# Optimization experiments

Measured on AMD Instinct MI355X. Metric: run time of the kernel, lower is better.

Reference implementation:

```python
import jax, jax.numpy as jnp
import numpy as np
import math

B, S, HID, H = 1, 2048, 1024, 16
D = HID // H  # head_dim = 64


def setup_inputs() -> dict:
    key = jax.random.key(0)
    ks = jax.random.split(key, 12)
    s = 0.02
    x = jax.random.normal(ks[0], (B, S, HID), jnp.float32)
    Wq = jax.random.normal(ks[1], (HID, HID), jnp.float32) * s
    bq = jnp.zeros((HID,), jnp.float32)
    Wk = jax.random.normal(ks[2], (HID, HID), jnp.float32) * s
    bk = jnp.zeros((HID,), jnp.float32)
    Wv = jax.random.normal(ks[3], (HID, HID), jnp.float32) * s
    bv = jnp.zeros((HID,), jnp.float32)
    Wo = jax.random.normal(ks[4], (HID, HID), jnp.float32) * s
    bo = jnp.zeros((HID,), jnp.float32)
    # nn.Parameter(torch.ones(3,3)) at init; small noise so the bias is non-degenerate
    cmw = jnp.ones((3, 3), jnp.float32) + 0.1 * jax.random.normal(ks[5], (3, 3), jnp.float32)
    # full causal [B,S,S] mask so the mask.shape[1]==seq_len branch is taken
    mask = jnp.tril(jnp.ones((B, S, S), jnp.int32))
    modality_info = jax.random.randint(ks[6], (B, S), 0, 3, dtype=jnp.int64)
    return dict(x=x, Wq=Wq, bq=bq, Wk=Wk, bk=bk, Wv=Wv, bv=bv, Wo=Wo, bo=bo,
                cmw=cmw, mask=mask, modality_info=modality_info)


def reference(x, Wq, bq, Wk, bk, Wv, bv, Wo, bo, cmw, mask, modality_info):
    b, s, _ = x.shape
    # QKV projections (torch Linear: y = x @ W.T + b), split into heads [B,H,S,D]
    q = (x @ Wq.T + bq).reshape(b, s, H, D).transpose(0, 2, 1, 3)
    k = (x @ Wk.T + bk).reshape(b, s, H, D).transpose(0, 2, 1, 3)
    v = (x @ Wv.T + bv).reshape(b, s, H, D).transpose(0, 2, 1, 3)
    scores = jnp.einsum('bhqd,bhkd->bhqk', q, k) / math.sqrt(D)  # [B,H,S,S]
    # cross-modal bias: gather from 3x3 table via pairwise modality indices -> [B,S,S]
    bias = cmw[modality_info[:, :, None], modality_info[:, None, :]]
    scores = scores + bias[:, None, :, :]  # equals original broadcast when B==1
    scores = jnp.where(mask[:, None, :, :] == 0, -1e9, scores)
    attn = jax.nn.softmax(scores, axis=-1)  # dropout is identity in eval
    ctx = jnp.einsum('bhqk,bhkd->bhqd', attn, v)          # [B,H,S,D]
    ctx = ctx.transpose(0, 2, 1, 3).reshape(b, s, HID)    # [B,S,HID]
    return ctx @ Wo.T + bo
```

## Files before the change

kernel.cpp:

```cpp
#include <hip/hip_runtime.h>
#include <hip/hip_bf16.h>
#include <math.h>

#define S_LEN 2048
#define HID   1024
#define NHEAD 16

using bf16x8 = __attribute__((ext_vector_type(8))) short;
using bf16x4 = __attribute__((ext_vector_type(4))) short;
using f32x4  = __attribute__((ext_vector_type(4))) float;

__device__ __forceinline__ float bf2f(short s) {
  union { unsigned u; float f; } c;
  c.u = ((unsigned)(unsigned short)s) << 16;
  return c.f;
}
__device__ __forceinline__ short f2bf(float f) {
  union { float f; unsigned u; } c; c.f = f;
  unsigned u = c.u;
  unsigned r = (u + 0x7fffu + ((u >> 16) & 1u)) >> 16;
  return (short)r;
}
__device__ __forceinline__ float loadf(const void* base, long idx, int is_bf) {
  return is_bf ? bf2f(((const short*)base)[idx]) : ((const float*)base)[idx];
}
__device__ __forceinline__ void gl_lds16(const void* g, void* l) {
  __builtin_amdgcn_global_load_lds(
      (const __attribute__((address_space(1))) void*)g,
      (__attribute__((address_space(3))) void*)l, 16, 0, 0);
}

__global__ __launch_bounds__(256) void convert5(
    const void* __restrict__ s0, const void* __restrict__ s1, const void* __restrict__ s2,
    const void* __restrict__ s3, const void* __restrict__ s4,
    short* __restrict__ d0, short* __restrict__ d1, short* __restrict__ d2,
    short* __restrict__ d3, short* __restrict__ d4,
    const int* __restrict__ modw, int* __restrict__ flags) {
  __shared__ int sh_isbf;
  const int t = threadIdx.x;

  if (t < 64) {
    const unsigned* xw = (const unsigned*)s0;
    int cnt = 0;
    for (int i = t; i < 1024; i += 64) {
      const unsigned fld = (xw[i] >> 7) & 0xFFu;
      cnt += (fld >= 100u && fld <= 135u) ? 1 : 0;
    }
    for (int m = 1; m < 64; m <<= 1) cnt += __shfl_xor(cnt, m);
    if (t == 0) sh_isbf = (cnt >= 512) ? 1 : 0;
  }
  __syncthreads();
  const int is_bf = sh_isbf;

  if (blockIdx.x == 0 && blockIdx.y == 0 && t < 64) {
    int odd = 0;
    for (int i = 0; i < 4; ++i) {
      const int wv = modw[2 * (t + 64 * i) + 1];
      odd += (wv != 0) ? 1 : 0;
    }
    for (int m = 1; m < 64; m <<= 1) odd += __shfl_xor(odd, m);
    if (t == 0) {
      flags[0] = is_bf;
      flags[1] = (odd == 0) ? 1 : 0;
    }
  }

  const int a = blockIdx.y;
  const void* src = (a == 0) ? s0 : (a == 1) ? s1 : (a == 2) ? s2 : (a == 3) ? s3 : s4;
  short* dst = (a == 0) ? d0 : (a == 1) ? d1 : (a == 2) ? d2 : (a == 3) ? d3 : d4;
  const long n = (a == 0) ? (2L << 20) : (1L << 20);
  long i = (long)(blockIdx.x * 256 + t) * 8;
  const long stride = (long)gridDim.x * 256 * 8;
  if (is_bf) {
    for (; i < n; i += stride)
      *(bf16x8*)(dst + i) = *(const bf16x8*)((const short*)src + i);
  } else {
    for (; i < n; i += stride) {
      const float* p = (const float*)src + i;
      bf16x8 r;
#pragma unroll
      for (int j = 0; j < 8; ++j) r[j] = f2bf(p[j]);
      *(bf16x8*)(dst + i) = r;
    }
  }
}

template <int BM, int BN>
__global__ __launch_bounds__(256) void gemm_bt3(
    const short* __restrict__ A,
    const short* __restrict__ W0, const short* __restrict__ W1, const short* __restrict__ W2,
    const void* __restrict__ b0, const void* __restrict__ b1, const void* __restrict__ b2,
    void* __restrict__ C0, void* __restrict__ C1, void* __restrict__ C2,
    const int* __restrict__ flags, int nbn, int store_f32)
{
  constexpr int K = 1024;
  constexpr int N = 1024;
  constexpr int NKT = K / 64;
  constexpr int WM = (BM == 128) ? 2 : 1;
  constexpr int WN = 4 / WM;
  constexpr int MI = (BM / 16) / WM;
  constexpr int NI = (BN / 16) / WN;
  constexpr int RPA = BM / 16;
  constexpr int RPB = BN / 16;
  __shared__ short As[2][2][BM * 32];
  __shared__ short Bs[2][2][BN * 32];

  const int t = threadIdx.x;
  const int w = t >> 6, lane = t & 63;
  const int l15 = lane & 15, quad = lane >> 4;
  const int wm = w / WN, wn = w % WN;
  const int is_bf = flags[0];

  const int mat = blockIdx.x / nbn;
  const int n0 = (blockIdx.x % nbn) * BN;
  const int m0 = blockIdx.y * BM;

  const short* W  = (mat == 0) ? W0 : (mat == 1 ? W1 : W2);
  const void* bia = (mat == 0) ? b0 : (mat == 1 ? b1 : b2);
  void*       C   = (mat == 0) ? C0 : (mat == 1 ? C1 : C2);

  f32x4 acc[MI][NI];
  for (int mi = 0; mi < MI; ++mi)
    for (int ni = 0; ni < NI; ++ni)
      for (int r = 0; r < 4; ++r) acc[mi][ni][r] = 0.f;

  const int srow = lane >> 2;
  const int sch  = (lane & 3) * 8;

  auto stage = [&](int kt, int buf) {
    for (int g = w; g < 2 * RPA; g += 4) {
      const int p = g / RPA, r0 = (g % RPA) * 16;
      gl_lds16(A + (long)(m0 + r0 + srow) * K + kt * 64 + p * 32 + sch,
               &As[buf][p][r0 * 32]);
    }
    for (int g = w; g < 2 * RPB; g += 4) {
      const int p = g / RPB, r0 = (g % RPB) * 16;
      gl_lds16(W + (long)(n0 + r0 + srow) * K + kt * 64 + p * 32 + sch,
               &Bs[buf][p][r0 * 32]);
    }
  };

  stage(0, 0);
  int cur = 0;
  for (int kt = 0; kt < NKT; ++kt) {
    __syncthreads();
    if (kt + 1 < NKT) stage(kt + 1, cur ^ 1);

    bf16x8 af[MI][2], bfr[NI][2];
    for (int p = 0; p < 2; ++p) {
      for (int mi = 0; mi < MI; ++mi)
        af[mi][p] = *(const bf16x8*)&As[cur][p][(wm * (MI * 16) + mi * 16 + l15) * 32 + quad * 8];
      for (int ni = 0; ni < NI; ++ni)
        bfr[ni][p] = *(const bf16x8*)&Bs[cur][p][(wn * (NI * 16) + ni * 16 + l15) * 32 + quad * 8];
    }
    for (int p = 0; p < 2; ++p)
      for (int mi = 0; mi < MI; ++mi)
        for (int ni = 0; ni < NI; ++ni)
          acc[mi][ni] = __builtin_amdgcn_mfma_f32_16x16x32_bf16(af[mi][p], bfr[ni][p], acc[mi][ni], 0, 0, 0);
    cur ^= 1;
  }

  for (int ni = 0; ni < NI; ++ni) {
    const int col = n0 + wn * (NI * 16) + ni * 16 + l15;
    const float bv = loadf(bia, col, is_bf);
    for (int mi = 0; mi < MI; ++mi) {
      const int row = m0 + wm * (MI * 16) + mi * 16 + quad * 4;
      for (int r = 0; r < 4; ++r) {
        const float v = acc[mi][ni][r] + bv;
        const long idx = (long)(row + r) * N + col;
        if (store_f32) ((float*)C)[idx] = v;
        else           ((short*)C)[idx] = f2bf(v);
      }
    }
  }
}

#define POSTRIDE (2L * 1024 * 1024)
__global__ __launch_bounds__(512) void attn_split(
    const short* __restrict__ Q, const short* __restrict__ Kg, const short* __restrict__ Vg,
    const int* __restrict__ mod, const void* __restrict__ cmw,
    const int* __restrict__ flags,
    short* __restrict__ PO, float* __restrict__ PL)
{
  __shared__ short Ks[64 * 80];
  __shared__ short Vt[64 * 80];
  __shared__ short Ps[8 * 16 * 80];
  __shared__ float cm[9];
  __shared__ int mods[2048];

  const int t = threadIdx.x;
  const int w = t >> 6, lane = t & 63;
  const int l15 = lane & 15, quad = lane >> 4;
  const int h = blockIdx.y;
  const int p   = blockIdx.x >> 2;
  const int par = blockIdx.x & 3;
  const int m64 = flags[1];
  const float KL2E = 0.125f * 1.44269504089f;

  if (t < 9) cm[t] = loadf(cmw, t, flags[0]) * 1.44269504089f;
  for (int i = t; i < 2048; i += 512) mods[i] = mod[i << m64];
  __syncthreads();

  short* POp = PO + (long)par * POSTRIDE;
  const int krow = t >> 3, kch = (t & 7) * 8;
  const int vkp = t & 63, vdc = (t >> 6) * 8;

  for (int si = 0; si < 2; ++si) {
    const int strip = si ? 15 - p : p;
    const int q0 = strip * 128;
    const int ktmax = 2 * strip + 1;
    const int qw0 = q0 + w * 16;

    const short* qb = Q + (long)(qw0 + l15) * HID + h * 64 + quad * 8;
    const bf16x8 aq0 = *(const bf16x8*)qb;
    const bf16x8 aq1 = *(const bf16x8*)(qb + 32);

    int mrow[4];
    for (int r = 0; r < 4; ++r) mrow[r] = mods[qw0 + quad * 4 + r];

    float lsum[4];
    f32x4 acc_o[4];
    for (int r = 0; r < 4; ++r) lsum[r] = 0.f;
    for (int ni = 0; ni < 4; ++ni)
      for (int r = 0; r < 4; ++r) acc_o[ni][r] = 0.f;

    bf16x8 rk, rv;
    auto preload = [&](int kt) {
      const long kb = (long)(kt * 64) * HID + h * 64;
      rk = *(const bf16x8*)(Kg + kb + (long)krow * HID + kch);
      rv = *(const bf16x8*)(Vg + kb + (long)vkp * HID + vdc);
    };

    if (par <= ktmax) {
      preload(par);
      for (int kt = par; kt <= ktmax; kt += 4) {
        __syncthreads();
        *(bf16x8*)&Ks[krow * 80 + kch] = rk;
#pragma unroll
        for (int j = 0; j < 8; ++j) Vt[(vdc + j) * 80 + vkp] = rv[j];
        __syncthreads();
        if (kt + 4 <= ktmax) preload(kt + 4);

        if (kt * 64 <= qw0 + 15) {
          f32x4 sc[4];
          __builtin_amdgcn_s_setprio(1);
          for (int nt = 0; nt < 4; ++nt) {
            const bf16x8 kb0 = *(const bf16x8*)&Ks[(nt * 16 + l15) * 80 + quad * 8];
            const bf16x8 kb1 = *(const bf16x8*)&Ks[(nt * 16 + l15) * 80 + 32 + quad * 8];
            f32x4 z;
            for (int r = 0; r < 4; ++r) z[r] = 0.f;
            z = __builtin_amdgcn_mfma_f32_16x16x32_bf16(aq0, kb0, z, 0, 0, 0);
            z = __builtin_amdgcn_mfma_f32_16x16x32_bf16(aq1, kb1, z, 0, 0, 0);
            sc[nt] = z;
          }
          __builtin_amdgcn_s_setprio(0);

          float sv[4][4];
          for (int nt = 0; nt < 4; ++nt) {
            const int mcol = mods[kt * 64 + nt * 16 + l15];
            for (int r = 0; r < 4; ++r)
              sv[nt][r] = sc[nt][r] * KL2E + cm[mrow[r] * 3 + mcol];
          }
          if (kt * 64 + 63 > qw0) {
            for (int nt = 0; nt < 4; ++nt) {
              const int col = kt * 64 + nt * 16 + l15;
              for (int r = 0; r < 4; ++r) {
                const int row = qw0 + quad * 4 + r;
                sv[nt][r] = (col <= row) ? sv[nt][r] : -1e30f;
              }
            }
          }
          short pb[4][4];
          for (int nt = 0; nt < 4; ++nt)
            for (int r = 0; r < 4; ++r) {
              const float pe = __builtin_exp2f(fminf(sv[nt][r], 86.56f));
              lsum[r] += pe;
              pb[nt][r] = f2bf(pe);
            }

          short* Pw = &Ps[w * 16 * 80];
          for (int nt = 0; nt < 4; ++nt)
            for (int r = 0; r < 4; ++r)
              Pw[(quad * 4 + r) * 80 + nt * 16 + l15] = pb[nt][r];
          asm volatile("s_waitcnt lgkmcnt(0)" ::: "memory");

          __builtin_amdgcn_s_setprio(1);
          for (int kk = 0; kk < 2; ++kk) {
            const bf16x8 ap = *(const bf16x8*)&Pw[l15 * 80 + kk * 32 + quad * 8];
            for (int ni = 0; ni < 4; ++ni) {
              const bf16x8 bv = *(const bf16x8*)&Vt[(ni * 16 + l15) * 80 + kk * 32 + quad * 8];
              acc_o[ni] = __builtin_amdgcn_mfma_f32_16x16x32_bf16(ap, bv, acc_o[ni], 0, 0, 0);
            }
          }
          __builtin_amdgcn_s_setprio(0);
        }
      }
    }

    for (int off = 1; off < 16; off <<= 1)
      for (int r = 0; r < 4; ++r) lsum[r] += __shfl_xor(lsum[r], off);

    for (int ni = 0; ni < 4; ++ni) {
      const int col = h * 64 + ni * 16 + l15;
      for (int r = 0; r < 4; ++r) {
        const int row = qw0 + quad * 4 + r;
        POp[(long)row * HID + col] = f2bf(acc_o[ni][r]);
      }
    }
    if (l15 == 0) {
      for (int r = 0; r < 4; ++r) {
        const int row = qw0 + quad * 4 + r;
        PL[par * 32768 + row * 16 + h] = lsum[r];
      }
    }
  }
}

__global__ __launch_bounds__(256) void attn_merge(
    const short* __restrict__ PO, const float* __restrict__ PL,
    short* __restrict__ CTX)
{
  const int row = blockIdx.x;
  const int t = threadIdx.x;
  const int h = t >> 4;
  const int d0 = (t & 15) * 4;
  float ls = 0.f;
#pragma unroll
  for (int i = 0; i < 4; ++i) ls += PL[i * 32768 + row * 16 + h];
  const float inv = 1.f / ls;
  const long b = (long)row * HID + h * 64 + d0;
  float o[4] = {0.f, 0.f, 0.f, 0.f};
#pragma unroll
  for (int i = 0; i < 4; ++i) {
    const bf16x4 v = *(const bf16x4*)&PO[i * POSTRIDE + b];
#pragma unroll
    for (int j = 0; j < 4; ++j) o[j] += bf2f(v[j]);
  }
  bf16x4 out;
#pragma unroll
  for (int j = 0; j < 4; ++j) out[j] = f2bf(o[j] * inv);
  *(bf16x4*)&CTX[b] = out;
}

extern "C" void kernel_launch(void* const* d_in, const int* in_sizes, int n_in,
                              void* d_out, int out_size, void* d_ws, size_t ws_size,
                              hipStream_t stream) {
  constexpr long M1 = 1024L * 1024L;
  int*   flags = (int*)d_ws;
  short* base  = (short*)d_ws + 128;
  short* xb  = base;
  short* Wqb = xb + 2 * M1;
  short* Wkb = Wqb + M1;
  short* Wvb = Wkb + M1;
  short* Wob = Wvb + M1;
  short* Qw  = Wob + M1;
  short* Kw  = Qw + 2 * M1;
  short* Vw  = Kw + 2 * M1;
  short* CTX = Vw + 2 * M1;
  short* PO4 = base + 14 * M1;
  float* PL4 = (float*)(base + 22 * M1);
  const int* modality = (const int*)d_in[11];

  convert5<<<dim3(512, 5), 256, 0, stream>>>(
      d_in[0], d_in[1], d_in[3], d_in[5], d_in[7],
      xb, Wqb, Wkb, Wvb, Wob, modality, flags);

  gemm_bt3<128, 64><<<dim3(48, 16), 256, 0, stream>>>(
      xb, Wqb, Wkb, Wvb, d_in[2], d_in[4], d_in[6],
      Qw, Kw, Vw, flags, 16, 0);
  attn_split<<<dim3(32, NHEAD), 512, 0, stream>>>(
      Qw, Kw, Vw, modality, d_in[9], flags, PO4, PL4);
  attn_merge<<<dim3(S_LEN), 256, 0, stream>>>(PO4, PL4, CTX);
  gemm_bt3<64, 64><<<dim3(16, 32), 256, 0, stream>>>(
      CTX, Wob, Wob, Wob, d_in[8], d_in[8], d_in[8],
      d_out, d_out, d_out, flags, 16, 1);
}
```

Baseline: 176.5 us.

## Load K fragments directly from global, double-buffer V in LDS

Each wave now reads its K MFMA operands straight from global memory into registers instead of staging K through shared memory. V's transposed tile goes into a double-buffered LDS array, which removes one of the two barriers per iteration. The LDS row padding changes from 80 to 88 shorts to alter bank mapping, and launch bounds now request 4 blocks per CU. This adds redundant global K reads across waves, exposes K load latency (no prefetch), and may increase register pressure under the new occupancy hint.

```diff
diff --git a/kernel.cpp b/kernel.cpp
--- a/kernel.cpp
+++ b/kernel.cpp
@@ -176,15 +176,14 @@
 }
 
 #define POSTRIDE (2L * 1024 * 1024)
-__global__ __launch_bounds__(512) void attn_split(
+__global__ __launch_bounds__(512, 4) void attn_split(
     const short* __restrict__ Q, const short* __restrict__ Kg, const short* __restrict__ Vg,
     const int* __restrict__ mod, const void* __restrict__ cmw,
     const int* __restrict__ flags,
     short* __restrict__ PO, float* __restrict__ PL)
 {
-  __shared__ short Ks[64 * 80];
-  __shared__ short Vt[64 * 80];
-  __shared__ short Ps[8 * 16 * 80];
+  __shared__ short Vt[2][64 * 88];
+  __shared__ short Ps[8 * 16 * 88];
   __shared__ float cm[9];
   __shared__ int mods[2048];
 
@@ -202,7 +201,6 @@
   __syncthreads();
 
   short* POp = PO + (long)par * POSTRIDE;
-  const int krow = t >> 3, kch = (t & 7) * 8;
   const int vkp = t & 63, vdc = (t >> 6) * 8;
 
   for (int si = 0; si < 2; ++si) {
@@ -224,33 +222,39 @@
     for (int ni = 0; ni < 4; ++ni)
       for (int r = 0; r < 4; ++r) acc_o[ni][r] = 0.f;
 
-    bf16x8 rk, rv;
-    auto preload = [&](int kt) {
-      const long kb = (long)(kt * 64) * HID + h * 64;
-      rk = *(const bf16x8*)(Kg + kb + (long)krow * HID + kch);
-      rv = *(const bf16x8*)(Vg + kb + (long)vkp * HID + vdc);
-    };
-
     if (par <= ktmax) {
-      preload(par);
+      bf16x8 rv = *(const bf16x8*)(Vg + (long)(par * 64) * HID + h * 64 +
+                                   (long)vkp * HID + vdc);
+      int cur = 0;
+      __syncthreads();
       for (int kt = par; kt <= ktmax; kt += 4) {
+        const bool act = (kt * 64 <= qw0 + 15);
+
+        bf16x8 kc0[4], kc1[4];
+        if (act) {
+          const short* kgb = Kg + (long)(kt * 64) * HID + h * 64;
+#pragma unroll
+          for (int nt = 0; nt < 4; ++nt) {
+            kc0[nt] = *(const bf16x8*)(kgb + (long)(nt * 16 + l15) * HID + quad * 8);
+            kc1[nt] = *(const bf16x8*)(kgb + (long)(nt * 16 + l15) * HID + 32 + quad * 8);
+          }
+        }
+
+#pragma unroll
+        for (int j = 0; j < 8; ++j) Vt[cur][(vdc + j) * 88 + vkp] = rv[j];
         __syncthreads();
-        *(bf16x8*)&Ks[krow * 80 + kch] = rk;
-#pragma unroll
-        for (int j = 0; j < 8; ++j) Vt[(vdc + j) * 80 + vkp] = rv[j];
-        __syncthreads();
-        if (kt + 4 <= ktmax) preload(kt + 4);
-
-        if (kt * 64 <= qw0 + 15) {
+        if (kt + 4 <= ktmax)
+          rv = *(const bf16x8*)(Vg + (long)((kt + 4) * 64) * HID + h * 64 +
+                                (long)vkp * HID + vdc);
+
+        if (act) {
           f32x4 sc[4];
           __builtin_amdgcn_s_setprio(1);
           for (int nt = 0; nt < 4; ++nt) {
-            const bf16x8 kb0 = *(const bf16x8*)&Ks[(nt * 16 + l15) * 80 + quad * 8];
-            const bf16x8 kb1 = *(const bf16x8*)&Ks[(nt * 16 + l15) * 80 + 32 + quad * 8];
             f32x4 z;
             for (int r = 0; r < 4; ++r) z[r] = 0.f;
-            z = __builtin_amdgcn_mfma_f32_16x16x32_bf16(aq0, kb0, z, 0, 0, 0);
-            z = __builtin_amdgcn_mfma_f32_16x16x32_bf16(aq1, kb1, z, 0, 0, 0);
+            z = __builtin_amdgcn_mfma_f32_16x16x32_bf16(aq0, kc0[nt], z, 0, 0, 0);
+            z = __builtin_amdgcn_mfma_f32_16x16x32_bf16(aq1, kc1[nt], z, 0, 0, 0);
             sc[nt] = z;
           }
           __builtin_amdgcn_s_setprio(0);
@@ -278,23 +282,26 @@
               pb[nt][r] = f2bf(pe);
             }
 
-          short* Pw = &Ps[w * 16 * 80];
+          short* Pw = &Ps[w * 16 * 88];
           for (int nt = 0; nt < 4; ++nt)
             for (int r = 0; r < 4; ++r)
-              Pw[(quad * 4 + r) * 80 + nt * 16 + l15] = pb[nt][r];
+              Pw[(quad * 4 + r) * 88 + nt * 16 + l15] = pb[nt][r];
           asm volatile("s_waitcnt lgkmcnt(0)" ::: "memory");
 
           __builtin_amdgcn_s_setprio(1);
           for (int kk = 0; kk < 2; ++kk) {
-            const bf16x8 ap = *(const bf16x8*)&Pw[l15 * 80 + kk * 32 + quad * 8];
+            const bf16x8 ap = *(const bf16x8*)&Pw[l15 * 88 + kk * 32 + quad * 8];
             for (int ni = 0; ni < 4; ++ni) {
-              const bf16x8 bv = *(const bf16x8*)&Vt[(ni * 16 + l15) * 80 + kk * 32 + quad * 8];
+              const bf16x8 bv = *(const bf16x8*)&Vt[cur][(ni * 16 + l15) * 88 + kk * 32 + quad * 8];
               acc_o[ni] = __builtin_amdgcn_mfma_f32_16x16x32_bf16(ap, bv, acc_o[ni], 0, 0, 0);
             }
           }
           __builtin_amdgcn_s_setprio(0);
         }
+        cur ^= 1;
       }
+    } else {
+      __syncthreads();
     }
 
     for (int off = 1; off < 16; off <<= 1)
```

Measured after the change: 220.8 us. +25.1%, slower.
